# Kernel optimization log

Measured on AMD Instinct MI355X. Metric: run time of the kernel, lower is better.

## Reference

```python
import jax, jax.numpy as jnp
import numpy as np

L = 2        # enc_depth
D = 1024     # enc_dim
HS = 1024    # hidden_size
NH = 16      # enc_heads
DH = 64      # dim_head
FF = 4096    # ff_mult * enc_dim
ROT = 32     # rotary dim = min(dim_head, 32)
B, SQ, SK = 64, 128, 512
EPS = 1e-8


def rmsnorm(x, w):
    # torch: x / clamp(||x||_2 * d**-0.5, eps) * w
    norm = jnp.sqrt(jnp.sum(x * x, axis=-1, keepdims=True)) * (x.shape[-1] ** -0.5)
    return x / jnp.maximum(norm, EPS) * w


def rope_freqs(n):
    inv_freq = 1.0 / (10000.0 ** (jnp.arange(0, ROT, 2, dtype=jnp.float32) / ROT))
    f = jnp.arange(n, dtype=jnp.float32)[:, None] * inv_freq[None, :]   # [n, ROT/2]
    return jnp.concatenate([f, f], axis=-1)[None, None]                  # [1,1,n,ROT]


def apply_rope(t, freqs):
    rd = freqs.shape[-1]
    t1, tp = t[..., :rd], t[..., rd:]
    half = rd // 2
    a, b = t1[..., :half], t1[..., half:]
    rot = jnp.concatenate([-b, a], axis=-1)
    t1 = t1 * jnp.cos(freqs) + rot * jnp.sin(freqs)
    return jnp.concatenate([t1, tp], axis=-1)


def attention(x, ctx, Wq, Wk, Wv, Wo, bo, pe_q, pe_k, mask):
    b, n, _ = x.shape
    m = ctx.shape[1]
    q = (x @ Wq).reshape(b, n, NH, DH).transpose(0, 2, 1, 3) * (DH ** -0.5)  # b h n d
    k = (ctx @ Wk).reshape(b, m, NH, DH).transpose(0, 2, 1, 3)
    v = (ctx @ Wv).reshape(b, m, NH, DH).transpose(0, 2, 1, 3)
    q = apply_rope(q, pe_q)
    k = apply_rope(k, pe_k)
    sim = jnp.einsum('bhid,bhjd->bhij', q, k)
    if mask is not None:
        sim = jnp.where(mask[:, None, None, :], sim, -jnp.finfo(sim.dtype).max)
    attn = jax.nn.softmax(sim, axis=-1)
    out = jnp.einsum('bhij,bhjd->bhid', attn, v)
    out = out.transpose(0, 2, 1, 3).reshape(b, n, NH * DH)
    return out @ Wo + bo


def setup_inputs() -> dict:
    key = jax.random.key(0)
    ks = jax.random.split(key, 24)
    s = 0.02
    inp = {
        'x': jax.random.normal(ks[0], (B, SQ, D), jnp.float32),
        'chunked_seq': jax.random.normal(ks[1], (B, SK, HS), jnp.float32),
        'mask': jnp.ones((B, SQ), dtype=bool),
        'attn_norm_w': jnp.ones((L, D), jnp.float32),
        'Wq': jax.random.normal(ks[2], (L, D, NH * DH), jnp.float32) * s,
        'Wk': jax.random.normal(ks[3], (L, D, NH * DH), jnp.float32) * s,
        'Wv': jax.random.normal(ks[4], (L, D, NH * DH), jnp.float32) * s,
        'Wo': jax.random.normal(ks[5], (L, NH * DH, D), jnp.float32) * s,
        'bo': jnp.zeros((L, D), jnp.float32),
        'cross_norm_w': jnp.ones((L, D), jnp.float32),
        'cWq': jax.random.normal(ks[6], (L, D, NH * DH), jnp.float32) * s,
        'cWk': jax.random.normal(ks[7], (HS, NH * DH), jnp.float32) * s if False else jax.random.normal(ks[7], (L, HS, NH * DH), jnp.float32) * s,
        'cWv': jax.random.normal(ks[8], (L, HS, NH * DH), jnp.float32) * s,
        'cWo': jax.random.normal(ks[9], (L, NH * DH, D), jnp.float32) * s,
        'cbo': jnp.zeros((L, D), jnp.float32),
        'ff_norm_w': jnp.ones((L, D), jnp.float32),
        'ff_w1': jax.random.normal(ks[10], (L, D, FF), jnp.float32) * s,
        'ff_b1': jnp.zeros((L, FF), jnp.float32),
        'ff_w2': jax.random.normal(ks[11], (L, FF, D), jnp.float32) * s,
        'ff_b2': jnp.zeros((L, D), jnp.float32),
        'norm_out_w': jnp.ones((D,), jnp.float32),
        'proj_w': jax.random.normal(ks[12], (D, HS), jnp.float32) * s,
        'proj_b': jnp.zeros((HS,), jnp.float32),
    }
    return inp


def reference(x, chunked_seq, mask, attn_norm_w, Wq, Wk, Wv, Wo, bo,
              cross_norm_w, cWq, cWk, cWv, cWo, cbo,
              ff_norm_w, ff_w1, ff_b1, ff_w2, ff_b2,
              norm_out_w, proj_w, proj_b):
    pe_q = rope_freqs(x.shape[-2])
    pe_k = rope_freqs(chunked_seq.shape[-2])
    for l in range(L):
        # PreNorm self-attention (RoPE on both q and k with q_pos_emb)
        h = rmsnorm(x, attn_norm_w[l])
        x = attention(h, h, Wq[l], Wk[l], Wv[l], Wo[l], bo[l], pe_q, pe_q, mask) + x
        # PreNorm cross-attention to chunked_seq (no mask)
        h = rmsnorm(x, cross_norm_w[l])
        x = attention(h, chunked_seq, cWq[l], cWk[l], cWv[l], cWo[l], cbo[l], pe_q, pe_k, None) + x
        # PreNorm feed-forward (exact GELU, as torch nn.GELU default)
        h = rmsnorm(x, ff_norm_w[l])
        x = (jax.nn.gelu(h @ ff_w1[l] + ff_b1[l], approximate=False) @ ff_w2[l] + ff_b2[l]) + x
    x = rmsnorm(x, norm_out_w)
    return x @ proj_w + proj_b
```

## Files before the change

kernel.cpp:

```cpp
#include <hip/hip_runtime.h>
#include <hip/hip_bf16.h>
#include <math.h>

typedef __hip_bfloat16 bf16;
typedef __bf16 bf16x8 __attribute__((ext_vector_type(8)));
typedef float f32x4 __attribute__((ext_vector_type(4)));

#define L_   2
#define D_   1024
#define NH_  16
#define DH_  64
#define FF_  4096
#define B_   64
#define SQ_  128
#define SK_  512
#define MTOK (B_ * SQ_)
#define MCTX (B_ * SK_)

#define GLDS16(gp, lp) __builtin_amdgcn_global_load_lds( \
    (__attribute__((address_space(1))) void*)(gp),        \
    (__attribute__((address_space(3))) void*)(lp), 16, 0, 0)

__global__ __launch_bounds__(256) void transpose_kernel(
    const float* __restrict__ in, bf16* __restrict__ out, int R, int C, float scale)
{
  __shared__ bf16 t[32][33];
  const int bx = blockIdx.x * 32;
  const int by = blockIdx.y * 32;
  const int tid = threadIdx.x;
#pragma unroll
  for (int e = 0; e < 4; ++e) {
    int i = tid + e * 256, rr = i >> 5, cc = i & 31;
    t[rr][cc] = __float2bfloat16(scale * in[(size_t)(by + rr) * C + bx + cc]);
  }
  __syncthreads();
#pragma unroll
  for (int e = 0; e < 4; ++e) {
    int i = tid + e * 256, rr = i >> 5, cc = i & 31;
    out[(size_t)(bx + rr) * R + by + cc] = t[cc][rr];
  }
}

__global__ __launch_bounds__(256) void convert_kernel(
    const float* __restrict__ in, bf16* __restrict__ out)
{
  const size_t i = ((size_t)blockIdx.x * 256 + threadIdx.x) * 8;
  const float4 f0 = *(const float4*)(in + i);
  const float4 f1 = *(const float4*)(in + i + 4);
  bf16x8 v = { (__bf16)f0.x, (__bf16)f0.y, (__bf16)f0.z, (__bf16)f0.w,
               (__bf16)f1.x, (__bf16)f1.y, (__bf16)f1.z, (__bf16)f1.w };
  *(bf16x8*)(out + i) = v;
}

__global__ __launch_bounds__(256) void rmsnorm_kernel(
    const float* __restrict__ x, const float* __restrict__ w, bf16* __restrict__ out)
{
  const int row = blockIdx.x, tid = threadIdx.x;
  const float4 v = ((const float4*)(x + (size_t)row * D_))[tid];
  float ss = v.x * v.x + v.y * v.y + v.z * v.z + v.w * v.w;
#pragma unroll
  for (int m = 1; m < 64; m <<= 1) ss += __shfl_xor(ss, m, 64);
  __shared__ float red[4];
  if ((tid & 63) == 0) red[tid >> 6] = ss;
  __syncthreads();
  const float tot = red[0] + red[1] + red[2] + red[3];
  const float inv = 1.0f / fmaxf(sqrtf(tot * (1.0f / D_)), 1e-8f);
  const float4 wv = ((const float4*)w)[tid];
  bf16* o = out + (size_t)row * D_ + tid * 4;
  o[0] = __float2bfloat16(v.x * inv * wv.x);
  o[1] = __float2bfloat16(v.y * inv * wv.y);
  o[2] = __float2bfloat16(v.z * inv * wv.z);
  o[3] = __float2bfloat16(v.w * inv * wv.w);
}

__global__ __launch_bounds__(256) void rope_kernel(bf16* __restrict__ t, int posmask, int ld)
{
  const int row = blockIdx.x, tid = threadIdx.x;
  const int h = tid >> 4, d = tid & 15;
  const float pos = (float)(row & posmask);
  const float inv_freq = expf(-(float)d * 0.5756462732485115f);
  const float f = pos * inv_freq;
  const float c = cosf(f), s = sinf(f);
  const size_t base = (size_t)row * ld + h * DH_ + d;
  const float a = __bfloat162float(t[base]);
  const float b = __bfloat162float(t[base + 16]);
  t[base]      = __float2bfloat16(a * c - b * s);
  t[base + 16] = __float2bfloat16(b * c + a * s);
}

template <int MODE, int AF32>
__global__ __launch_bounds__(256) void gemm_bt_kernel(
    const void* __restrict__ Ap, const bf16* __restrict__ Bt,
    void* Cout, const float* __restrict__ bias, const float* resid,
    int M, int N, int K)
{
  __shared__ __align__(16) bf16 As[128 * 32];
  __shared__ __align__(16) bf16 Bs[128 * 32];
  const int tid = threadIdx.x;
  const int wave = tid >> 6, lane = tid & 63;
  const int wm = wave >> 1, wn = wave & 1;

  const int npidn = gridDim.x, npidm = gridDim.y;
  const int pid = blockIdx.y * npidn + blockIdx.x;
  const int group_sz = 8 * npidn;
  const int gid = pid / group_sz;
  const int first_m = gid * 8;
  const int gsm = min(npidm - first_m, 8);
  const int pid_m = first_m + (pid % gsm);
  const int pid_n = (pid % group_sz) / gsm;
  const int m0 = pid_m * 128, n0 = pid_n * 128;

  const int r = lane & 15, qd = lane >> 4;
  const int srow = lane >> 2, scol = (lane & 3) * 8;

  f32x4 acc[4][4] = {};

  for (int k0 = 0; k0 < K; k0 += 32) {
#pragma unroll
    for (int t = 0; t < 2; ++t) {
      const int g = wave * 2 + t;
      if (AF32) {
        const float* A32 = (const float*)Ap;
        const float4 f0 = *(const float4*)(A32 + (size_t)(m0 + g * 16 + srow) * K + k0 + scol);
        const float4 f1 = *(const float4*)(A32 + (size_t)(m0 + g * 16 + srow) * K + k0 + scol + 4);
        bf16x8 v = { (__bf16)f0.x, (__bf16)f0.y, (__bf16)f0.z, (__bf16)f0.w,
                     (__bf16)f1.x, (__bf16)f1.y, (__bf16)f1.z, (__bf16)f1.w };
        *(bf16x8*)&As[g * 512 + lane * 8] = v;
      } else {
        const bf16* A16 = (const bf16*)Ap;
        GLDS16(A16 + (size_t)(m0 + g * 16 + srow) * K + k0 + scol, &As[g * 512]);
      }
      GLDS16(Bt + (size_t)(n0 + g * 16 + srow) * K + k0 + scol, &Bs[g * 512]);
    }
    __syncthreads();
    bf16x8 af[4], bfr[4];
#pragma unroll
    for (int i = 0; i < 4; ++i)
      af[i] = *(const bf16x8*)&As[(wm * 64 + i * 16 + r) * 32 + qd * 8];
#pragma unroll
    for (int j = 0; j < 4; ++j)
      bfr[j] = *(const bf16x8*)&Bs[(wn * 64 + j * 16 + r) * 32 + qd * 8];
#pragma unroll
    for (int i = 0; i < 4; ++i)
#pragma unroll
      for (int j = 0; j < 4; ++j)
        acc[i][j] = __builtin_amdgcn_mfma_f32_16x16x32_bf16(af[i], bfr[j], acc[i][j], 0, 0, 0);
    __syncthreads();
  }

#pragma unroll
  for (int i = 0; i < 4; ++i) {
    const int row = m0 + wm * 64 + i * 16 + qd * 4;
#pragma unroll
    for (int j = 0; j < 4; ++j) {
      const int col = n0 + wn * 64 + j * 16 + r;
      const float bv = bias ? bias[col] : 0.f;
#pragma unroll
      for (int rr = 0; rr < 4; ++rr) {
        float v = acc[i][j][rr] + bv;
        const size_t idx = (size_t)(row + rr) * N + col;
        if (MODE == 0) {
          ((bf16*)Cout)[idx] = __float2bfloat16(v);
        } else if (MODE == 1) {
          v = 0.5f * v * (1.f + erff(v * 0.70710678118654752f));
          ((bf16*)Cout)[idx] = __float2bfloat16(v);
        } else if (MODE == 2) {
          ((float*)Cout)[idx] = v + resid[idx];
        } else {
          ((float*)Cout)[idx] = v;
        }
      }
    }
  }
}

__global__ __launch_bounds__(256) void attn_kernel(
    const bf16* __restrict__ Q, const bf16* __restrict__ Kg,
    const bf16* __restrict__ Vg, bf16* __restrict__ Out,
    int nk, int ldq, int ldkv)
{
  __shared__ __align__(16) bf16 Qs[128 * 64];
  __shared__ __align__(16) bf16 Ks[64 * 64];
  __shared__ __align__(16) bf16 Vt[64 * 64];
  __shared__ __align__(16) bf16 Ps[128 * 64];
  const int tid = threadIdx.x;
  const int wave = tid >> 6, lane = tid & 63;
  const int b = blockIdx.x >> 4, h = blockIdx.x & 15;
  const int r = lane & 15, qd = lane >> 4;
  const int srow = lane >> 3;
  const int scol = ((lane & 7) ^ srow) * 8;

#pragma unroll
  for (int t = 0; t < 4; ++t) {
    const int g = wave * 4 + t;
    GLDS16(Q + (size_t)(b * SQ_ + g * 8 + srow) * ldq + h * DH_ + scol, &Qs[g * 512]);
  }

  float mrow[2][4], lrow[2][4];
  f32x4 Oacc[2][4] = {};
#pragma unroll
  for (int i = 0; i < 2; ++i)
#pragma unroll
    for (int rr = 0; rr < 4; ++rr) { mrow[i][rr] = -1e30f; lrow[i][rr] = 0.f; }

  for (int kt = 0; kt < nk; kt += 64) {
#pragma unroll
    for (int t = 0; t < 2; ++t) {
      const int g = wave * 2 + t;
      GLDS16(Kg + (size_t)(b * nk + kt + g * 8 + srow) * ldkv + h * DH_ + scol, &Ks[g * 512]);
    }
#pragma unroll
    for (int c = 0; c < 2; ++c) {
      const int chunk = c * 256 + tid;
      const int key = chunk >> 3, d0 = (chunk & 7) * 8;
      const uint4 pv = *(const uint4*)(Vg + (size_t)(b * nk + kt + key) * ldkv + h * DH_ + d0);
      const unsigned short* pu = (const unsigned short*)&pv;
      const int s0 = key >> 3, k7 = key & 7;
#pragma unroll
      for (int t2 = 0; t2 < 8; ++t2) {
        const int row = d0 + t2;
        ((unsigned short*)Vt)[row * 64 + ((s0 ^ (row & 7)) << 3) + k7] = pu[t2];
      }
    }
    __syncthreads();

    f32x4 S[2][4] = {};
#pragma unroll
    for (int ks = 0; ks < 2; ++ks) {
      const int sl = ((ks * 4 + qd) ^ (r & 7)) * 8;
      bf16x8 aq[2], bk[4];
#pragma unroll
      for (int i = 0; i < 2; ++i)
        aq[i] = *(const bf16x8*)&Qs[(wave * 32 + i * 16 + r) * 64 + sl];
#pragma unroll
      for (int j = 0; j < 4; ++j)
        bk[j] = *(const bf16x8*)&Ks[(j * 16 + r) * 64 + sl];
#pragma unroll
      for (int i = 0; i < 2; ++i)
#pragma unroll
        for (int j = 0; j < 4; ++j)
          S[i][j] = __builtin_amdgcn_mfma_f32_16x16x32_bf16(aq[i], bk[j], S[i][j], 0, 0, 0);
    }

#pragma unroll
    for (int i = 0; i < 2; ++i) {
#pragma unroll
      for (int rr = 0; rr < 4; ++rr) {
        float mx = fmaxf(fmaxf(S[i][0][rr], S[i][1][rr]), fmaxf(S[i][2][rr], S[i][3][rr]));
#pragma unroll
        for (int mm = 1; mm < 16; mm <<= 1) mx = fmaxf(mx, __shfl_xor(mx, mm, 64));
        const float mnew = fmaxf(mrow[i][rr], mx);
        const float alpha = __expf(mrow[i][rr] - mnew);
        mrow[i][rr] = mnew;
        const int prow = wave * 32 + i * 16 + qd * 4 + rr;
        const int pr7 = prow & 7;
        float rs = 0.f;
#pragma unroll
        for (int j = 0; j < 4; ++j) {
          const float p = __expf(S[i][j][rr] - mnew);
          rs += p;
          Ps[prow * 64 + (((j * 2 + (r >> 3)) ^ pr7) << 3) + (r & 7)] = __float2bfloat16(p);
        }
#pragma unroll
        for (int mm = 1; mm < 16; mm <<= 1) rs += __shfl_xor(rs, mm, 64);
        lrow[i][rr] = lrow[i][rr] * alpha + rs;
#pragma unroll
        for (int jd = 0; jd < 4; ++jd) Oacc[i][jd][rr] *= alpha;
      }
    }
    __syncthreads();

#pragma unroll
    for (int ks = 0; ks < 2; ++ks) {
      const int sl = ((ks * 4 + qd) ^ (r & 7)) * 8;
      bf16x8 ap[2], bv[4];
#pragma unroll
      for (int i = 0; i < 2; ++i)
        ap[i] = *(const bf16x8*)&Ps[(wave * 32 + i * 16 + r) * 64 + sl];
#pragma unroll
      for (int jd = 0; jd < 4; ++jd)
        bv[jd] = *(const bf16x8*)&Vt[(jd * 16 + r) * 64 + sl];
#pragma unroll
      for (int i = 0; i < 2; ++i)
#pragma unroll
        for (int jd = 0; jd < 4; ++jd)
          Oacc[i][jd] = __builtin_amdgcn_mfma_f32_16x16x32_bf16(ap[i], bv[jd], Oacc[i][jd], 0, 0, 0);
    }
    __syncthreads();
  }

#pragma unroll
  for (int i = 0; i < 2; ++i) {
    const int rowl = wave * 32 + i * 16 + qd * 4;
#pragma unroll
    for (int jd = 0; jd < 4; ++jd) {
      const int col = h * DH_ + jd * 16 + r;
#pragma unroll
      for (int rr = 0; rr < 4; ++rr)
        Out[(size_t)(b * SQ_ + rowl + rr) * D_ + col] =
            __float2bfloat16(Oacc[i][jd][rr] / lrow[i][rr]);
    }
  }
}

extern "C" void kernel_launch(void* const* d_in, const int* in_sizes, int n_in,
                              void* d_out, int out_size, void* d_ws, size_t ws_size,
                              hipStream_t stream)
{
  (void)in_sizes; (void)n_in; (void)out_size;
  const float* x_in         = (const float*)d_in[0];
  const float* ctx          = (const float*)d_in[1];
  const float* attn_norm_w  = (const float*)d_in[3];
  const float* Wq           = (const float*)d_in[4];
  const float* Wk           = (const float*)d_in[5];
  const float* Wv           = (const float*)d_in[6];
  const float* Wo           = (const float*)d_in[7];
  const float* bo           = (const float*)d_in[8];
  const float* cross_norm_w = (const float*)d_in[9];
  const float* cWq          = (const float*)d_in[10];
  const float* cWk          = (const float*)d_in[11];
  const float* cWv          = (const float*)d_in[12];
  const float* cWo          = (const float*)d_in[13];
  const float* cbo          = (const float*)d_in[14];
  const float* ff_norm_w    = (const float*)d_in[15];
  const float* ff_w1        = (const float*)d_in[16];
  const float* ff_b1        = (const float*)d_in[17];
  const float* ff_w2        = (const float*)d_in[18];
  const float* ff_b2        = (const float*)d_in[19];
  const float* norm_out_w   = (const float*)d_in[20];
  const float* proj_w       = (const float*)d_in[21];
  const float* proj_b       = (const float*)d_in[22];

  char* ws = (char*)d_ws;
  size_t off = 0;
  auto carve = [&](size_t bytes) -> void* {
    void* p = ws + off;
    off += (bytes + 255) & ~(size_t)255;
    return p;
  };
  const size_t DD = (size_t)D_ * D_;
  bf16*  Wt  = (bf16*)carve((size_t)FF_ * D_ * 2);
  float* xf  = (float*)carve((size_t)MTOK * D_ * 4);
  bf16*  hb  = (bf16*)carve((size_t)MTOK * D_ * 2);
  bf16*  ao  = hb;
  char*  big = (char*)carve((size_t)144 * 1024 * 1024);
  bf16*  qkvb = (bf16*)big;
  bf16*  qb   = (bf16*)big;
  bf16*  kvb  = (bf16*)(big + (size_t)16 * 1024 * 1024);
  bf16*  gbuf = (bf16*)big;
  bf16*  ctxb = (bf16*)carve((size_t)MCTX * D_ * 2);
  const bool ctx16 = (ws_size >= off);

  auto T = [&](const float* src, bf16* dst, int R, int C, float scale = 1.0f) {
    transpose_kernel<<<dim3(C / 32, R / 32), 256, 0, stream>>>(src, dst, R, C, scale);
  };
  auto G0 = [&](const bf16* A, bf16* C, int M, int N, int K) {
    gemm_bt_kernel<0, 0><<<dim3(N / 128, M / 128), 256, 0, stream>>>(
        (const void*)A, Wt, (void*)C, nullptr, nullptr, M, N, K);
  };
  auto G0f = [&](const float* A, bf16* C, int M, int N, int K) {
    gemm_bt_kernel<0, 1><<<dim3(N / 128, M / 128), 256, 0, stream>>>(
        (const void*)A, Wt, (void*)C, nullptr, nullptr, M, N, K);
  };
  auto G1 = [&](const bf16* A, bf16* C, const float* bias, int M, int N, int K) {
    gemm_bt_kernel<1, 0><<<dim3(N / 128, M / 128), 256, 0, stream>>>(
        (const void*)A, Wt, (void*)C, bias, nullptr, M, N, K);
  };
  auto G2 = [&](const bf16* A, const float* bias, const float* resid, int M, int N, int K) {
    gemm_bt_kernel<2, 0><<<dim3(N / 128, M / 128), 256, 0, stream>>>(
        (const void*)A, Wt, (void*)xf, bias, resid, M, N, K);
  };
  auto G3 = [&](const bf16* A, float* C, const float* bias, int M, int N, int K) {
    gemm_bt_kernel<3, 0><<<dim3(N / 128, M / 128), 256, 0, stream>>>(
        (const void*)A, Wt, (void*)C, bias, nullptr, M, N, K);
  };

  if (ctx16)
    convert_kernel<<<(MCTX * D_) / (256 * 8), 256, 0, stream>>>(ctx, ctxb);

  for (int l = 0; l < L_; ++l) {
    const size_t o1 = (size_t)l * DD;
    const size_t o4 = (size_t)l * D_ * FF_;
    const float* res0 = (l == 0) ? x_in : xf;
    rmsnorm_kernel<<<MTOK, 256, 0, stream>>>(res0, attn_norm_w + l * D_, hb);
    T(Wq + o1, Wt,          D_, D_, 0.125f);
    T(Wk + o1, Wt + DD,     D_, D_);
    T(Wv + o1, Wt + 2 * DD, D_, D_);
    G0(hb, qkvb, MTOK, 3 * D_, D_);
    rope_kernel<<<MTOK, 256, 0, stream>>>(qkvb,        SQ_ - 1, 3 * D_);
    rope_kernel<<<MTOK, 256, 0, stream>>>(qkvb + D_,   SQ_ - 1, 3 * D_);
    attn_kernel<<<B_ * NH_, 256, 0, stream>>>(qkvb, qkvb + D_, qkvb + 2 * D_, ao,
                                              SQ_, 3 * D_, 3 * D_);
    T(Wo + o1, Wt, D_, D_);
    G2(ao, bo + l * D_, res0, MTOK, D_, D_);
    rmsnorm_kernel<<<MTOK, 256, 0, stream>>>(xf, cross_norm_w + l * D_, hb);
    T(cWq + o1, Wt, D_, D_, 0.125f);
    G0(hb, qb, MTOK, D_, D_);
    T(cWk + o1, Wt,      D_, D_);
    T(cWv + o1, Wt + DD, D_, D_);
    if (ctx16) G0(ctxb, kvb, MCTX, 2 * D_, D_);
    else       G0f(ctx, kvb, MCTX, 2 * D_, D_);
    rope_kernel<<<MTOK, 256, 0, stream>>>(qb,  SQ_ - 1, D_);
    rope_kernel<<<MCTX, 256, 0, stream>>>(kvb, SK_ - 1, 2 * D_);
    attn_kernel<<<B_ * NH_, 256, 0, stream>>>(qb, kvb, kvb + D_, ao, SK_, D_, 2 * D_);
    T(cWo + o1, Wt, D_, D_);
    G2(ao, cbo + l * D_, xf, MTOK, D_, D_);
    rmsnorm_kernel<<<MTOK, 256, 0, stream>>>(xf, ff_norm_w + l * D_, hb);
    T(ff_w1 + o4, Wt, D_, FF_);
    G1(hb, gbuf, ff_b1 + l * FF_, MTOK, FF_, D_);
    T(ff_w2 + o4, Wt, FF_, D_);
    G2(gbuf, ff_b2 + l * D_, xf, MTOK, D_, FF_);
  }
  rmsnorm_kernel<<<MTOK, 256, 0, stream>>>(xf, norm_out_w, hb);
  T(proj_w, Wt, D_, D_);
  G3(hb, (float*)d_out, proj_b, MTOK, D_, D_);
}
```

Baseline: 2.139 ms.

## Double GEMM K-tile to 64 and stage bf16 epilogue through LDS

Result: slower. 2.225 ms (+4.1%).

```diff
diff --git a/kernel.cpp b/kernel.cpp
--- a/kernel.cpp
+++ b/kernel.cpp
@@ -94,8 +94,10 @@
     void* Cout, const float* __restrict__ bias, const float* resid,
     int M, int N, int K)
 {
-  __shared__ __align__(16) bf16 As[128 * 32];
-  __shared__ __align__(16) bf16 Bs[128 * 32];
+  __shared__ __align__(16) char smem[34816];
+  bf16* As = (bf16*)smem;
+  bf16* Bs = (bf16*)(smem + 16384);
+  bf16* Cs = (bf16*)smem;
   const int tid = threadIdx.x;
   const int wave = tid >> 6, lane = tid & 63;
   const int wm = wave >> 1, wn = wave & 1;
@@ -111,63 +113,83 @@
   const int m0 = pid_m * 128, n0 = pid_n * 128;
 
   const int r = lane & 15, qd = lane >> 4;
-  const int srow = lane >> 2, scol = (lane & 3) * 8;
+  const int srow = lane >> 3, scol = (lane & 7) * 8;
 
   f32x4 acc[4][4] = {};
 
-  for (int k0 = 0; k0 < K; k0 += 32) {
-#pragma unroll
-    for (int t = 0; t < 2; ++t) {
-      const int g = wave * 2 + t;
+  for (int k0 = 0; k0 < K; k0 += 64) {
+#pragma unroll
+    for (int t = 0; t < 4; ++t) {
+      const int g = wave * 4 + t;
       if (AF32) {
         const float* A32 = (const float*)Ap;
-        const float4 f0 = *(const float4*)(A32 + (size_t)(m0 + g * 16 + srow) * K + k0 + scol);
-        const float4 f1 = *(const float4*)(A32 + (size_t)(m0 + g * 16 + srow) * K + k0 + scol + 4);
+        const float4 f0 = *(const float4*)(A32 + (size_t)(m0 + g * 8 + srow) * K + k0 + scol);
+        const float4 f1 = *(const float4*)(A32 + (size_t)(m0 + g * 8 + srow) * K + k0 + scol + 4);
         bf16x8 v = { (__bf16)f0.x, (__bf16)f0.y, (__bf16)f0.z, (__bf16)f0.w,
                      (__bf16)f1.x, (__bf16)f1.y, (__bf16)f1.z, (__bf16)f1.w };
         *(bf16x8*)&As[g * 512 + lane * 8] = v;
       } else {
         const bf16* A16 = (const bf16*)Ap;
-        GLDS16(A16 + (size_t)(m0 + g * 16 + srow) * K + k0 + scol, &As[g * 512]);
+        GLDS16(A16 + (size_t)(m0 + g * 8 + srow) * K + k0 + scol, &As[g * 512]);
       }
-      GLDS16(Bt + (size_t)(n0 + g * 16 + srow) * K + k0 + scol, &Bs[g * 512]);
-    }
-    __syncthreads();
-    bf16x8 af[4], bfr[4];
-#pragma unroll
-    for (int i = 0; i < 4; ++i)
-      af[i] = *(const bf16x8*)&As[(wm * 64 + i * 16 + r) * 32 + qd * 8];
-#pragma unroll
-    for (int j = 0; j < 4; ++j)
-      bfr[j] = *(const bf16x8*)&Bs[(wn * 64 + j * 16 + r) * 32 + qd * 8];
-#pragma unroll
-    for (int i = 0; i < 4; ++i)
+      GLDS16(Bt + (size_t)(n0 + g * 8 + srow) * K + k0 + scol, &Bs[g * 512]);
+    }
+    __syncthreads();
+#pragma unroll
+    for (int kk = 0; kk < 2; ++kk) {
+      bf16x8 af[4], bfr[4];
+#pragma unroll
+      for (int i = 0; i < 4; ++i)
+        af[i] = *(const bf16x8*)&As[(wm * 64 + i * 16 + r) * 64 + kk * 32 + qd * 8];
 #pragma unroll
       for (int j = 0; j < 4; ++j)
-        acc[i][j] = __builtin_amdgcn_mfma_f32_16x16x32_bf16(af[i], bfr[j], acc[i][j], 0, 0, 0);
-    __syncthreads();
-  }
-
-#pragma unroll
-  for (int i = 0; i < 4; ++i) {
-    const int row = m0 + wm * 64 + i * 16 + qd * 4;
-#pragma unroll
-    for (int j = 0; j < 4; ++j) {
-      const int col = n0 + wn * 64 + j * 16 + r;
-      const float bv = bias ? bias[col] : 0.f;
-#pragma unroll
-      for (int rr = 0; rr < 4; ++rr) {
-        float v = acc[i][j][rr] + bv;
-        const size_t idx = (size_t)(row + rr) * N + col;
-        if (MODE == 0) {
-          ((bf16*)Cout)[idx] = __float2bfloat16(v);
-        } else if (MODE == 1) {
-          v = 0.5f * v * (1.f + erff(v * 0.70710678118654752f));
-          ((bf16*)Cout)[idx] = __float2bfloat16(v);
-        } else if (MODE == 2) {
-          ((float*)Cout)[idx] = v + resid[idx];
-        } else {
-          ((float*)Cout)[idx] = v;
+        bfr[j] = *(const bf16x8*)&Bs[(wn * 64 + j * 16 + r) * 64 + kk * 32 + qd * 8];
+#pragma unroll
+      for (int i = 0; i < 4; ++i)
+#pragma unroll
+        for (int j = 0; j < 4; ++j)
+          acc[i][j] = __builtin_amdgcn_mfma_f32_16x16x32_bf16(af[i], bfr[j], acc[i][j], 0, 0, 0);
+    }
+    __syncthreads();
+  }
+
+  if (MODE == 0 || MODE == 1) {
+#pragma unroll
+    for (int i = 0; i < 4; ++i) {
+#pragma unroll
+      for (int j = 0; j < 4; ++j) {
+        const int col = wn * 64 + j * 16 + r;
+        const float bv = bias ? bias[n0 + col] : 0.f;
+#pragma unroll
+        for (int rr = 0; rr < 4; ++rr) {
+          float v = acc[i][j][rr] + bv;
+          if (MODE == 1) v = 0.5f * v * (1.f + erff(v * 0.70710678118654752f));
+          Cs[(wm * 64 + i * 16 + qd * 4 + rr) * 136 + col] = __float2bfloat16(v);
+        }
+      }
+    }
+    __syncthreads();
+    const int orow = tid >> 4, ocol = (tid & 15) * 8;
+#pragma unroll
+    for (int rd = 0; rd < 8; ++rd) {
+      const int rrow = rd * 16 + orow;
+      const bf16x8 v = *(const bf16x8*)&Cs[rrow * 136 + ocol];
+      *(bf16x8*)((bf16*)Cout + (size_t)(m0 + rrow) * N + n0 + ocol) = v;
+    }
+  } else {
+#pragma unroll
+    for (int i = 0; i < 4; ++i) {
+      const int row = m0 + wm * 64 + i * 16 + qd * 4;
+#pragma unroll
+      for (int j = 0; j < 4; ++j) {
+        const int col = n0 + wn * 64 + j * 16 + r;
+        const float bv = bias ? bias[col] : 0.f;
+#pragma unroll
+        for (int rr = 0; rr < 4; ++rr) {
+          float v = acc[i][j][rr] + bv;
+          const size_t idx = (size_t)(row + rr) * N + col;
+          if (MODE == 2) ((float*)Cout)[idx] = v + resid[idx];
+          else           ((float*)Cout)[idx] = v;
         }
       }
     }
```
